# Kernel tuning notes

Hardware: AMD Instinct MI355X
Metric: run time of the kernel (lower is better)

The kernel has to match this reference:

```python
import jax, jax.numpy as jnp
import numpy as np

LOG2PI = float(np.log(2.0 * np.pi))
MIN_DURATION = 1
NUM_STATES = 512
OBS_DIM = 128
B, T, K = 64, 2000, 400


def setup_inputs() -> dict:
    key = jax.random.key(0)
    ks = jax.random.split(key, 10)
    observations = jax.random.normal(ks[0], (B, T, OBS_DIM), dtype=jnp.float32)
    state_sequence = jax.random.randint(ks[1], (B, K), 0, NUM_STATES, dtype=jnp.int32)
    # durations >= min_duration so gamma log-prob stays finite
    duration_sequence = jax.random.randint(ks[2], (B, K), 1, 51, dtype=jnp.int32)
    # learned parameters, initialized as in the torch module
    alpha_params = jnp.ones((NUM_STATES,), jnp.float32)
    beta_params = jnp.ones((NUM_STATES,), jnp.float32)
    transition_logits = jax.random.normal(ks[3], (NUM_STATES, NUM_STATES), dtype=jnp.float32)
    initial_logits = jnp.zeros((NUM_STATES,), jnp.float32)
    observation_means = jax.random.normal(ks[4], (NUM_STATES, OBS_DIM), dtype=jnp.float32)
    observation_logvars = jnp.zeros((NUM_STATES, OBS_DIM), jnp.float32)
    return {
        "observations": observations,
        "alpha_params": alpha_params,
        "beta_params": beta_params,
        "transition_logits": transition_logits,
        "initial_logits": initial_logits,
        "observation_means": observation_means,
        "observation_logvars": observation_logvars,
        "state_sequence": state_sequence,
        "duration_sequence": duration_sequence,
    }


def _gamma_duration_logprob(alpha_params, beta_params, state_sequence, duration_sequence):
    # fully vectorized version of the per-sample Python loop in DurationModel
    d = duration_sequence.astype(jnp.float32)                      # [B, K]
    alpha = jax.nn.softplus(alpha_params)[state_sequence] + 1e-6   # [B, K]
    beta = jax.nn.softplus(beta_params)[state_sequence] + 1e-6
    lp = (alpha - 1.0) * jnp.log(d + 1e-8) - beta * d
    lp = lp - (jax.lax.lgamma(alpha) - alpha * jnp.log(beta))
    return jnp.where(d >= MIN_DURATION, lp, -jnp.inf)


def reference(observations, alpha_params, beta_params, transition_logits,
              initial_logits, observation_means, observation_logvars,
              state_sequence, duration_sequence):
    # --- duration log-probs per segment: [B, K]
    log_dur = _gamma_duration_logprob(alpha_params, beta_params,
                                      state_sequence, duration_sequence)

    # --- expand segments to frames: frame t belongs to segment with cum[idx-1] <= t < cum[idx]
    cum = jnp.cumsum(duration_sequence, axis=1)                    # [B, K]
    t = jnp.arange(observations.shape[1])                          # [T]
    seg_idx = jax.vmap(lambda c: jnp.searchsorted(c, t, side='right'))(cum)
    seg_idx = jnp.clip(seg_idx, 0, state_sequence.shape[1] - 1)    # [B, T]
    frame_states = jnp.take_along_axis(state_sequence, seg_idx, axis=1)  # [B, T]

    # --- diagonal-gaussian observation log-probs per frame: [B, T]
    mu = observation_means[frame_states]                           # [B, T, D]
    lv = observation_logvars[frame_states]                         # [B, T, D]
    resid2 = (observations - mu) ** 2 * jnp.exp(-lv)
    log_obs = -0.5 * jnp.sum(lv + resid2 + LOG2PI, axis=-1)        # [B, T]

    # --- initial + transition log-probs over the segment-level state chain
    log_trans = jax.nn.log_softmax(transition_logits, axis=-1)     # [S, S]
    log_init = jax.nn.log_softmax(initial_logits)                  # [S]
    trans_lp = log_trans[state_sequence[:, :-1], state_sequence[:, 1:]].sum(axis=1)  # [B]
    init_lp = log_init[state_sequence[:, 0]]                       # [B]

    # --- per-sequence supervised log-likelihood: [B]
    log_likelihood = log_obs.sum(axis=1) + log_dur.sum(axis=1) + trans_lp + init_lp
    return log_likelihood
```

## Files before the change

kernel.cpp:

```cpp
#include <hip/hip_runtime.h>
#include <hip/hip_bf16.h>
#include <math.h>

#define NS 512
#define OD 128
#define BB 64
#define TT 2000
#define KK 400
#define CHUNK 64
#define NCH 32
#define LOG2PI_F 1.8378770664093453f
#define SEQ_OFF  576
#define PART_OFF 1024


__device__ __forceinline__ float softplusf(float x) {
    return (x > 20.f) ? x : log1pf(expf(x));
}

__global__ __launch_bounds__(256) void big_kernel(
    const float* __restrict__ obs, const float* __restrict__ mu,
    const float* __restrict__ lvar, const float* __restrict__ trans,
    const float* __restrict__ init_logits,
    const float* __restrict__ alpha_p, const float* __restrict__ beta_p,
    const int* __restrict__ states, const int* __restrict__ durs,
    float* __restrict__ ws)
{
    const int tid = threadIdx.x;
    const int bid = blockIdx.x;
    __shared__ float red[4];

    if (bid < BB * NCH) {
        const int b = bid >> 5;
        const int t0 = (bid & 31) * CHUNK;

        __shared__ int st[KK];
        __shared__ int cum[512];
        __shared__ int csum[8];
        __shared__ int fsl[CHUNK];

        const int lane = tid & 63, w = tid >> 6;
        int v0 = 0, v1 = 0;
        if (tid < KK) { st[tid] = states[b * KK + tid]; v0 = durs[b * KK + tid]; }
        if (tid + 256 < KK) { st[tid + 256] = states[b * KK + tid + 256];
                              v1 = durs[b * KK + tid + 256]; }
        #pragma unroll
        for (int off = 1; off < 64; off <<= 1) {
            int u0 = __shfl_up(v0, off, 64);
            int u1 = __shfl_up(v1, off, 64);
            if (lane >= off) { v0 += u0; v1 += u1; }
        }
        if (lane == 63) { csum[w] = v0; csum[4 + w] = v1; }
        __syncthreads();
        int off0 = 0, off1 = 0;
        #pragma unroll
        for (int c = 0; c < 8; ++c) {
            int cs = csum[c];
            off0 += (c < w) ? cs : 0;
            off1 += (c < 4 + w) ? cs : 0;
        }
        cum[tid] = v0 + off0;
        cum[tid + 256] = v1 + off1;
        __syncthreads();

        if (tid < CHUNK) {
            const int t = t0 + tid;
            int lo = 0, hi = KK;
            while (lo < hi) {
                int mid = (lo + hi) >> 1;
                if (cum[mid] <= t) lo = mid + 1; else hi = mid;
            }
            fsl[tid] = st[(lo > KK - 1) ? (KK - 1) : lo];
        }
        __syncthreads();

        const int row = tid >> 5;
        const int d = (tid & 31) * 4;
        float acc = 0.f;
        if (t0 + CHUNK <= TT) {
            #pragma unroll
            for (int i = 0; i < CHUNK / 8; ++i) {
                const int t = t0 + i * 8 + row;
                const int s = fsl[i * 8 + row];
                const float4 o  = *(const float4*)(obs + ((size_t)(b * TT + t)) * OD + d);
                const float4 m  = *(const float4*)(mu  + (size_t)s * OD + d);
                const float4 lv = *(const float4*)(lvar + (size_t)s * OD + d);
                const float dx = o.x - m.x, dy = o.y - m.y, dz = o.z - m.z, dw = o.w - m.w;
                acc += lv.x + lv.y + lv.z + lv.w + 4.f * LOG2PI_F
                     + dx * dx * __expf(-lv.x) + dy * dy * __expf(-lv.y)
                     + dz * dz * __expf(-lv.z) + dw * dw * __expf(-lv.w);
            }
        } else {
            #pragma unroll
            for (int i = 0; i < CHUNK / 8; ++i) {
                const int t = t0 + i * 8 + row;
                if (t < TT) {
                    const int s = fsl[i * 8 + row];
                    const float4 o  = *(const float4*)(obs + ((size_t)(b * TT + t)) * OD + d);
                    const float4 m  = *(const float4*)(mu  + (size_t)s * OD + d);
                    const float4 lv = *(const float4*)(lvar + (size_t)s * OD + d);
                    const float dx = o.x - m.x, dy = o.y - m.y, dz = o.z - m.z, dw = o.w - m.w;
                    acc += lv.x + lv.y + lv.z + lv.w + 4.f * LOG2PI_F
                         + dx * dx * __expf(-lv.x) + dy * dy * __expf(-lv.y)
                         + dz * dz * __expf(-lv.z) + dw * dw * __expf(-lv.w);
                }
            }
        }
        for (int off = 32; off; off >>= 1) acc += __shfl_down(acc, off, 64);
        if ((tid & 63) == 0) red[tid >> 6] = acc;
        __syncthreads();
        if (tid == 0)
            ws[PART_OFF + bid] = -0.5f * (red[0] + red[1] + red[2] + red[3]);
    } else if (bid < BB * NCH + NS + 1) {
        const int r = bid - BB * NCH;
        const float* src = (r < NS) ? (trans + (size_t)r * NS) : init_logits;
        float x0 = src[tid];
        float x1 = src[tid + 256];
        float m = fmaxf(x0, x1);
        for (int off = 32; off; off >>= 1) m = fmaxf(m, __shfl_down(m, off, 64));
        if ((tid & 63) == 0) red[tid >> 6] = m;
        __syncthreads();
        m = fmaxf(fmaxf(red[0], red[1]), fmaxf(red[2], red[3]));
        __syncthreads();
        float e = __expf(x0 - m) + __expf(x1 - m);
        for (int off = 32; off; off >>= 1) e += __shfl_down(e, off, 64);
        if ((tid & 63) == 0) red[tid >> 6] = e;
        __syncthreads();
        if (tid == 0)
            ws[(r < NS) ? r : 512] = m + __logf(red[0] + red[1] + red[2] + red[3]);
    } else {
        const int b = bid - (BB * NCH + NS + 1);
        float lp = 0.f;
        for (int k = tid; k < KK; k += 256) {
            const int s = states[b * KK + k];
            const float dv = (float)durs[b * KK + k];
            const float a  = softplusf(alpha_p[s]) + 1e-6f;
            const float bt = softplusf(beta_p[s]) + 1e-6f;
            float v = (a - 1.f) * __logf(dv + 1e-8f) - bt * dv
                    + a * __logf(bt) - lgammaf(a);
            lp += (dv >= 1.f) ? v : -INFINITY;
            if (k < KK - 1)
                lp += trans[(size_t)s * NS + states[b * KK + k + 1]];
        }
        for (int off = 32; off; off >>= 1) lp += __shfl_down(lp, off, 64);
        if ((tid & 63) == 0) red[tid >> 6] = lp;
        __syncthreads();
        if (tid == 0)
            ws[SEQ_OFF + b] = red[0] + red[1] + red[2] + red[3]
                            + init_logits[states[b * KK]];
    }
}

__global__ __launch_bounds__(256) void fin_kernel(
    const int* __restrict__ states, const float* __restrict__ ws,
    float* __restrict__ out)
{
    const int b = blockIdx.x;
    const int tid = threadIdx.x;
    __shared__ float red[4];

    float lp = 0.f;
    if (tid < NCH)       lp = ws[PART_OFF + b * NCH + tid];
    else if (tid == NCH) lp = ws[SEQ_OFF + b] - ws[512];
    for (int k = tid; k < KK - 1; k += 256)
        lp -= ws[states[b * KK + k]];
    for (int off = 32; off; off >>= 1) lp += __shfl_down(lp, off, 64);
    if ((tid & 63) == 0) red[tid >> 6] = lp;
    __syncthreads();
    if (tid == 0)
        out[b] = red[0] + red[1] + red[2] + red[3];
}

extern "C" void kernel_launch(void* const* d_in, const int* in_sizes, int n_in,
                              void* d_out, int out_size, void* d_ws, size_t ws_size,
                              hipStream_t stream) {
    const float* observations = (const float*)d_in[0];
    const float* alpha_p      = (const float*)d_in[1];
    const float* beta_p       = (const float*)d_in[2];
    const float* trans        = (const float*)d_in[3];
    const float* init_logits  = (const float*)d_in[4];
    const float* obs_means    = (const float*)d_in[5];
    const float* obs_logvars  = (const float*)d_in[6];
    const int*   state_seq    = (const int*)d_in[7];
    const int*   dur_seq      = (const int*)d_in[8];

    float* ws = (float*)d_ws;
    float* out = (float*)d_out;

    big_kernel<<<BB * NCH + NS + 1 + BB, 256, 0, stream>>>(
        observations, obs_means, obs_logvars, trans, init_logits,
        alpha_p, beta_p, state_seq, dur_seq, ws);
    fin_kernel<<<BB, 256, 0, stream>>>(state_seq, ws, out);
}
```

Before: 24.30 us.

## Replace per-frame binary search with segment scatter fill and double chunk size

Each thread now holds its segment's state and its cumulative end in registers and writes that state directly into the frame-to-state table for the frames it covers in the chunk. This replaces the shared-memory cumulative array and the per-frame binary search, removing one barrier and a serial log-depth search. The last segment is stretched to the end of the chunk to match the clipping in the reference. The chunk size is also doubled, which halves the number of observation blocks and spreads the per-block prefix-scan overhead over more frames, at the cost of fewer blocks for latency hiding.

```diff
diff --git a/kernel.cpp b/kernel.cpp
--- a/kernel.cpp
+++ b/kernel.cpp
@@ -7,8 +7,8 @@
 #define BB 64
 #define TT 2000
 #define KK 400
-#define CHUNK 64
-#define NCH 32
+#define CHUNK 128
+#define NCH 16
 #define LOG2PI_F 1.8378770664093453f
 #define SEQ_OFF  576
 #define PART_OFF 1024
@@ -31,19 +31,21 @@
     __shared__ float red[4];
 
     if (bid < BB * NCH) {
-        const int b = bid >> 5;
-        const int t0 = (bid & 31) * CHUNK;
+        const int b = bid >> 4;
+        const int t0 = (bid & 15) * CHUNK;
 
-        __shared__ int st[KK];
-        __shared__ int cum[512];
+        __shared__ int fsl[CHUNK];
         __shared__ int csum[8];
-        __shared__ int fsl[CHUNK];
 
         const int lane = tid & 63, w = tid >> 6;
-        int v0 = 0, v1 = 0;
-        if (tid < KK) { st[tid] = states[b * KK + tid]; v0 = durs[b * KK + tid]; }
-        if (tid + 256 < KK) { st[tid + 256] = states[b * KK + tid + 256];
-                              v1 = durs[b * KK + tid + 256]; }
+        int s0v = 0, d0 = 0, s1v = 0, d1 = 0;
+        s0v = states[b * KK + tid];
+        d0  = durs[b * KK + tid];
+        if (tid + 256 < KK) {
+            s1v = states[b * KK + tid + 256];
+            d1  = durs[b * KK + tid + 256];
+        }
+        int v0 = d0, v1 = d1;
         #pragma unroll
         for (int off = 1; off < 64; off <<= 1) {
             int u0 = __shfl_up(v0, off, 64);
@@ -59,18 +61,18 @@
             off0 += (c < w) ? cs : 0;
             off1 += (c < 4 + w) ? cs : 0;
         }
-        cum[tid] = v0 + off0;
-        cum[tid + 256] = v1 + off1;
-        __syncthreads();
+        const int c0 = v0 + off0;
+        const int c1 = v1 + off1;
 
-        if (tid < CHUNK) {
-            const int t = t0 + tid;
-            int lo = 0, hi = KK;
-            while (lo < hi) {
-                int mid = (lo + hi) >> 1;
-                if (cum[mid] <= t) lo = mid + 1; else hi = mid;
-            }
-            fsl[tid] = st[(lo > KK - 1) ? (KK - 1) : lo];
+        {
+            int a = c0 - d0, e = c0;
+            a = (a < t0) ? t0 : a;
+            e = (e > t0 + CHUNK) ? t0 + CHUNK : e;
+            for (int t = a; t < e; ++t) fsl[t - t0] = s0v;
+            int a1 = c1 - d1, e1 = (tid + 256 == KK - 1) ? t0 + CHUNK : c1;
+            a1 = (a1 < t0) ? t0 : a1;
+            e1 = (e1 > t0 + CHUNK) ? t0 + CHUNK : e1;
+            for (int t = a1; t < e1; ++t) fsl[t - t0] = s1v;
         }
         __syncthreads();
 
```

After: 23.27 us. 4.3% less time.
